# Kernel optimization log

Measured on AMD Instinct MI355X. Metric: run time of the kernel, lower is better.

Reference implementation:

```python
import jax, jax.numpy as jnp
import numpy as np

S, B, H, NH = 2048, 1, 1024, 16
HD = H // NH  # 64
NEG = float(np.finfo(np.float16).min)  # masked_fill value, matches torch.finfo(torch.float16).min


def setup_inputs() -> dict:
    key = jax.random.key(0)
    ks = jax.random.split(key, 9)
    w = lambda k: jax.random.normal(k, (H, H), jnp.float32) * 0.02
    b = lambda k: jax.random.normal(k, (H,), jnp.float32) * 0.01
    # causal (left-to-right) boolean mask, True = keep
    mask = jnp.tril(jnp.ones((S, S), dtype=bool))[None, None]  # [1,1,S,S]
    return {
        "hidden_states": jax.random.normal(ks[0], (S, B, H), jnp.float32),
        "Wq": w(ks[1]), "bq": b(ks[2]),
        "Wk": w(ks[3]), "bk": b(ks[4]),
        "Wv": w(ks[5]), "bv": b(ks[6]),
        "Wo": w(ks[7]), "bo": b(ks[8]),
        "attention_mask": mask,
    }


def reference(hidden_states, Wq, bq, Wk, bk, Wv, bv, Wo, bo, attention_mask):
    s, bsz, h = hidden_states.shape
    norm = float(np.sqrt(HD))
    # QKV projections (nn.Linear: x @ W.T + b), reshape to [S, B, NH, HD]
    q = (hidden_states @ Wq.T + bq).reshape(s, bsz, NH, HD) / norm
    k = (hidden_states @ Wk.T + bk).reshape(s, bsz, NH, HD)
    v = (hidden_states @ Wv.T + bv).reshape(s, bsz, NH, HD)
    # scores: [B, NH, S_q, S_kv] (baddbmm equivalent)
    scores = jnp.einsum('sbhd,tbhd->bhst', q, k)
    scores = jnp.where(attention_mask, scores, jnp.asarray(NEG, scores.dtype))
    # fp32 softmax, cast back to score dtype
    probs = jax.nn.softmax(scores.astype(jnp.float32), axis=-1).astype(scores.dtype)
    # context: [S, B, NH, HD] -> [S, B, H]
    ctx = jnp.einsum('bhst,tbhd->sbhd', probs, v).reshape(s, bsz, h)
    out = ctx @ Wo.T + bo
    return out
```

## Files before the change

kernel.cpp:

```cpp
#include <hip/hip_runtime.h>

typedef __attribute__((ext_vector_type(8))) short bf16x8;
typedef __attribute__((ext_vector_type(8))) unsigned short u16x8;
typedef __attribute__((ext_vector_type(4))) float f32x4;

#define GLDS16(SRC, DST) __builtin_amdgcn_global_load_lds( \
    (const __attribute__((address_space(1))) void*)(SRC),  \
    (__attribute__((address_space(3))) void*)(DST), 16, 0, 0)

__device__ __forceinline__ unsigned short f2bf(float f) {
  unsigned int u = __float_as_uint(f);
  u += 0x7FFFu + ((u >> 16) & 1u);
  return (unsigned short)(u >> 16);
}
__device__ __forceinline__ float bf2f(unsigned short u) {
  return __uint_as_float((unsigned int)u << 16);
}

__global__ void cvt_all(const float* __restrict__ hid,
                        const float* __restrict__ Wq, const float* __restrict__ Wk,
                        const float* __restrict__ Wv, const float* __restrict__ Wo,
                        const float* __restrict__ bq, const float* __restrict__ bk,
                        const float* __restrict__ bv,
                        unsigned short* __restrict__ hb, unsigned short* __restrict__ Wcat,
                        unsigned short* __restrict__ Wob, float* __restrict__ bcat) {
  const int H4 = 2048 * 1024 / 4, W4 = 1024 * 1024 / 4;
  int i = blockIdx.x * 256 + threadIdx.x;
  const float* src; unsigned short* dst; float scale = 1.0f; int j;
  if (i < H4)                { src = hid; dst = hb;                 j = i; }
  else if (i < H4 + W4)      { src = Wq;  dst = Wcat;               j = i - H4; scale = 0.125f; }
  else if (i < H4 + 2 * W4)  { src = Wk;  dst = Wcat + 1024 * 1024; j = i - H4 - W4; }
  else if (i < H4 + 3 * W4)  { src = Wv;  dst = Wcat + 2048 * 1024; j = i - H4 - 2 * W4; }
  else if (i < H4 + 4 * W4)  { src = Wo;  dst = Wob;                j = i - H4 - 3 * W4; }
  else {
    j = i - H4 - 4 * W4;
    int e = j * 4;
    const float* b = (e < 1024) ? bq : (e < 2048 ? bk + (-1024) : bv + (-2048));
    float4 v = *(const float4*)(b + e);
    if (e < 1024) { v.x *= 0.125f; v.y *= 0.125f; v.z *= 0.125f; v.w *= 0.125f; }
    ((float4*)bcat)[j] = v;
    return;
  }
  float4 v = ((const float4*)src)[j];
  ushort4 o;
  o.x = f2bf(v.x * scale); o.y = f2bf(v.y * scale);
  o.z = f2bf(v.z * scale); o.w = f2bf(v.w * scale);
  ((ushort4*)dst)[j] = o;
}

template <int BM, int BN, typename OutT>
__global__ __launch_bounds__(256) void gemm_bt(
    const unsigned short* __restrict__ A, const unsigned short* __restrict__ B,
    const float* __restrict__ bias, OutT* __restrict__ C,
    int M, int N, int K, int lda, int ldb, int ldc)
{
  constexpr int MREP = BM / 32, NREP = BN / 32;
  __shared__ __align__(16) unsigned short As[2][BM * 32];
  __shared__ __align__(16) unsigned short Bs[2][BN * 32];
  const int t = threadIdx.x;
  const int lane = t & 63;
  const int w = t >> 6;
  const int wm = w >> 1, wn = w & 1;
  const int lr = lane & 15, lk = lane >> 4;
  const int tm = blockIdx.y * BM, tn = blockIdx.x * BN;

  f32x4 acc[MREP][NREP];
#pragma unroll
  for (int m = 0; m < MREP; ++m)
#pragma unroll
    for (int n = 0; n < NREP; ++n) acc[m][n] = (f32x4){0.f, 0.f, 0.f, 0.f};

  const int ra0 = t >> 2;
  const int ka0 = (t & 3) << 3;
  const int ra1 = 64 + (t >> 2);
  const int lds0 = (t & 192) * 8;
  const int lds1 = (256 + (t & 192)) * 8;

  const int NT = K >> 5;
  GLDS16(A + (size_t)(tm + ra0) * lda + ka0, &As[0][lds0]);
  if constexpr (BM == 128) GLDS16(A + (size_t)(tm + ra1) * lda + ka0, &As[0][lds1]);
  GLDS16(B + (size_t)(tn + ra0) * ldb + ka0, &Bs[0][lds0]);
  if constexpr (BN == 128) GLDS16(B + (size_t)(tn + ra1) * ldb + ka0, &Bs[0][lds1]);
  __syncthreads();

  for (int kt = 0; kt < NT; ++kt) {
    const int cur = kt & 1, nxt = cur ^ 1;
    if (kt + 1 < NT) {
      const int k0 = (kt + 1) << 5;
      GLDS16(A + (size_t)(tm + ra0) * lda + k0 + ka0, &As[nxt][lds0]);
      if constexpr (BM == 128) GLDS16(A + (size_t)(tm + ra1) * lda + k0 + ka0, &As[nxt][lds1]);
      GLDS16(B + (size_t)(tn + ra0) * ldb + k0 + ka0, &Bs[nxt][lds0]);
      if constexpr (BN == 128) GLDS16(B + (size_t)(tn + ra1) * ldb + k0 + ka0, &Bs[nxt][lds1]);
    }
    bf16x8 af[MREP], bfv[NREP];
#pragma unroll
    for (int m = 0; m < MREP; ++m)
      af[m] = *(const bf16x8*)&As[cur][(wm * (BM / 2) + m * 16 + lr) * 32 + lk * 8];
#pragma unroll
    for (int n = 0; n < NREP; ++n)
      bfv[n] = *(const bf16x8*)&Bs[cur][(wn * (BN / 2) + n * 16 + lr) * 32 + lk * 8];
#pragma unroll
    for (int m = 0; m < MREP; ++m)
#pragma unroll
      for (int n = 0; n < NREP; ++n)
        acc[m][n] = __builtin_amdgcn_mfma_f32_16x16x32_bf16(af[m], bfv[n], acc[m][n], 0, 0, 0);
    __syncthreads();
  }

#pragma unroll
  for (int m = 0; m < MREP; ++m) {
    const int row0 = tm + wm * (BM / 2) + m * 16 + lk * 4;
#pragma unroll
    for (int n = 0; n < NREP; ++n) {
      const int col = tn + wn * (BN / 2) + n * 16 + lr;
      const float bb = bias ? bias[col] : 0.f;
#pragma unroll
      for (int r = 0; r < 4; ++r) {
        float v = acc[m][n][r] + bb;
        if constexpr (sizeof(OutT) == 2) {
          ((unsigned short*)C)[(size_t)(row0 + r) * ldc + col] = f2bf(v);
        } else {
          ((float*)C)[(size_t)(row0 + r) * ldc + col] = v;
        }
      }
    }
  }
}

__device__ __forceinline__ int slot_off(int qt) {
  int g = qt >> 3;
  return (g == 1) ? (qt - 8) * 2 : (g == 2) ? 16 + (qt - 16) * 3 : 40 + (qt - 24) * 4;
}

__global__ __launch_bounds__(256) void attn_fwd(const unsigned short* __restrict__ QKV,
                                                unsigned short* __restrict__ ctx,
                                                unsigned short* __restrict__ Opart,
                                                float* __restrict__ mlbuf)
{
  __shared__ __align__(16) unsigned short Ks[64 * 64];
  __shared__ __align__(16) unsigned short Vt[64 * 64];
  __shared__ __align__(16) unsigned int   Pl[4][16 * 36];

  const int t = threadIdx.x;
  const int lane = t & 63, w = t >> 6;
  const int lr = lane & 15, lk = lane >> 4;
  const int h = blockIdx.y;
  const int p = 79 - (int)blockIdx.x;
  int qt, c;
  if (p < 8)       { qt = p; c = 0; }
  else if (p < 24) { qt = 8 + ((p - 8) >> 1); c = (p - 8) & 1; }
  else if (p < 48) { int r = p - 24; qt = 16 + r / 3; c = r - (r / 3) * 3; }
  else             { int r = p - 48; qt = 24 + (r >> 2); c = r & 3; }
  const int nc = (qt >> 3) + 1;
  const int q0 = qt * 64;
  const size_t ldq = 3072;

  const unsigned short* qbase = QKV + (size_t)(q0 + w * 16 + lr) * ldq + h * 64;
  const bf16x8 qf0 = *(const bf16x8*)(qbase + lk * 8);
  const bf16x8 qf1 = *(const bf16x8*)(qbase + 32 + lk * 8);

  f32x4 acc[4];
#pragma unroll
  for (int d = 0; d < 4; ++d) acc[d] = (f32x4){0.f, 0.f, 0.f, 0.f};
  float mrun = -__builtin_inff(), lrun = 0.f;

  const int srow0 = t >> 3;
  const int srow1 = 32 + (t >> 3);
  const int sslot = t & 7;

  const unsigned short* kbase = QKV + 1024 + h * 64;
  const unsigned short* vbase = QKV + 2048 + h * 64;

  const int kt0 = c * 8;
  const int kt1 = (qt < kt0 + 7) ? qt : kt0 + 7;
  for (int kt = kt0; kt <= kt1; ++kt) {
    const int kv0 = kt * 64;
    __syncthreads();
    {
      const int c0 = (sslot ^ (srow0 & 7)) << 3;
      const int c1 = (sslot ^ (srow1 & 7)) << 3;
      GLDS16(kbase + (size_t)(kv0 + srow0) * ldq + c0, &Ks[(t & 192) * 8]);
      GLDS16(kbase + (size_t)(kv0 + srow1) * ldq + c1, &Ks[(256 + (t & 192)) * 8]);
    }
    {
      const bf16x8 v0 = *(const bf16x8*)(vbase + (size_t)(kv0 + srow0) * ldq + (sslot << 3));
      const bf16x8 v1 = *(const bf16x8*)(vbase + (size_t)(kv0 + srow1) * ldq + (sslot << 3));
      const int d0 = sslot << 3;
#pragma unroll
      for (int j = 0; j < 8; ++j) {
        const int d = d0 + j;
        const int key = (d ^ (d >> 3)) & 7;
        Vt[d * 64 + (((srow0 >> 3) ^ key) << 3) + (srow0 & 7)] = (unsigned short)v0[j];
        Vt[d * 64 + (((srow1 >> 3) ^ key) << 3) + (srow1 & 7)] = (unsigned short)v1[j];
      }
    }
    __syncthreads();

    f32x4 sacc[4];
#pragma unroll
    for (int sub = 0; sub < 4; ++sub) {
      const int krow = sub * 16 + lr;
      const int sw = krow & 7;
      const bf16x8 kf0 = *(const bf16x8*)&Ks[krow * 64 + ((lk ^ sw) << 3)];
      const bf16x8 kf1 = *(const bf16x8*)&Ks[krow * 64 + (((4 + lk) ^ sw) << 3)];
      f32x4 s = (f32x4){0.f, 0.f, 0.f, 0.f};
      s = __builtin_amdgcn_mfma_f32_16x16x32_bf16(kf0, qf0, s, 0, 0, 0);
      s = __builtin_amdgcn_mfma_f32_16x16x32_bf16(kf1, qf1, s, 0, 0, 0);
      sacc[sub] = s;
    }

    if (kt == qt) {
      const int qg = w * 16 + lr;
#pragma unroll
      for (int sub = 0; sub < 4; ++sub) {
#pragma unroll
        for (int r = 0; r < 4; ++r)
          if (sub * 16 + lk * 4 + r > qg) sacc[sub][r] = -__builtin_inff();
      }
    }

    float pm = -__builtin_inff();
#pragma unroll
    for (int sub = 0; sub < 4; ++sub)
#pragma unroll
      for (int r = 0; r < 4; ++r) pm = fmaxf(pm, sacc[sub][r]);
    pm = fmaxf(pm, __shfl_xor(pm, 16, 64));
    pm = fmaxf(pm, __shfl_xor(pm, 32, 64));
    const float mnew = fmaxf(mrun, pm);
    const float sc = __expf(mrun - mnew);
    lrun *= sc;
#pragma unroll
    for (int d = 0; d < 4; ++d) acc[d] *= sc;
    float pp[4][4]; float rs = 0.f;
#pragma unroll
    for (int sub = 0; sub < 4; ++sub)
#pragma unroll
      for (int r = 0; r < 4; ++r) { pp[sub][r] = __expf(sacc[sub][r] - mnew); rs += pp[sub][r]; }
    rs += __shfl_xor(rs, 16, 64);
    rs += __shfl_xor(rs, 32, 64);
    lrun += rs;
    mrun = mnew;

    unsigned int* prow = &Pl[w][lr * 36];
#pragma unroll
    for (int sub = 0; sub < 4; ++sub) {
#pragma unroll
      for (int j = 0; j < 2; ++j) {
        unsigned int pk;
        asm("v_cvt_pk_bf16_f32 %0, %1, %2" : "=v"(pk) : "v"(pp[sub][2 * j]), "v"(pp[sub][2 * j + 1]));
        prow[sub * 8 + lk * 2 + j] = pk;
      }
    }
    asm volatile("s_waitcnt lgkmcnt(0)" ::: "memory");
    __builtin_amdgcn_sched_barrier(0);

    const bf16x8 pb0 = *(const bf16x8*)&Pl[w][lr * 36 + lk * 4];
    const bf16x8 pb1 = *(const bf16x8*)&Pl[w][lr * 36 + 16 + lk * 4];
#pragma unroll
    for (int dsub = 0; dsub < 4; ++dsub) {
      const int dd = dsub * 16 + lr;
      const int key = (dd ^ (dd >> 3)) & 7;
      const bf16x8 bv0 = *(const bf16x8*)&Vt[dd * 64 + ((lk ^ key) << 3)];
      const bf16x8 bv1 = *(const bf16x8*)&Vt[dd * 64 + (((4 + lk) ^ key) << 3)];
      acc[dsub] = __builtin_amdgcn_mfma_f32_16x16x32_bf16(bv0, pb0, acc[dsub], 0, 0, 0);
      acc[dsub] = __builtin_amdgcn_mfma_f32_16x16x32_bf16(bv1, pb1, acc[dsub], 0, 0, 0);
    }
  }

  if (nc == 1) {
    const float inv = 1.0f / lrun;
#pragma unroll
    for (int dsub = 0; dsub < 4; ++dsub) {
      ushort4 o;
      o.x = f2bf(acc[dsub][0] * inv);
      o.y = f2bf(acc[dsub][1] * inv);
      o.z = f2bf(acc[dsub][2] * inv);
      o.w = f2bf(acc[dsub][3] * inv);
      *(ushort4*)&ctx[(size_t)(q0 + w * 16 + lr) * 1024 + h * 64 + dsub * 16 + lk * 4] = o;
    }
  } else {
    const int slot = h * 72 + slot_off(qt) + c;
    unsigned short* Op = Opart + (size_t)slot * 4096;
    const int ql = w * 16 + lr;
#pragma unroll
    for (int dsub = 0; dsub < 4; ++dsub) {
      ushort4 o;
      o.x = f2bf(acc[dsub][0]);
      o.y = f2bf(acc[dsub][1]);
      o.z = f2bf(acc[dsub][2]);
      o.w = f2bf(acc[dsub][3]);
      *(ushort4*)&Op[ql * 64 + dsub * 16 + lk * 4] = o;
    }
    if (lk == 0)
      *(float2*)&mlbuf[(slot * 64 + ql) * 2] = make_float2(mrun, lrun);
  }
}

template <int NC>
__device__ __forceinline__ void combine_body(const unsigned short* __restrict__ Opart,
                                             const float* __restrict__ mlbuf,
                                             unsigned short* __restrict__ ctx,
                                             int qt, int half, int h, int t) {
  const int q = half * 32 + (t >> 3);
  const int d0 = (t & 7) * 8;
  const int slot0 = h * 72 + slot_off(qt);
  float m[NC], l[NC];
#pragma unroll
  for (int c = 0; c < NC; ++c) {
    const float2 ml = *(const float2*)&mlbuf[((slot0 + c) * 64 + q) * 2];
    m[c] = ml.x; l[c] = ml.y;
  }
  float M = m[0];
#pragma unroll
  for (int c = 1; c < NC; ++c) M = fmaxf(M, m[c]);
  float wgt[NC], L = 0.f;
#pragma unroll
  for (int c = 0; c < NC; ++c) { wgt[c] = __expf(m[c] - M); L += wgt[c] * l[c]; }
  u16x8 v[NC];
#pragma unroll
  for (int c = 0; c < NC; ++c)
    v[c] = *(const u16x8*)&Opart[(size_t)(slot0 + c) * 4096 + q * 64 + d0];
  const float inv = 1.0f / L;
  u16x8 r;
#pragma unroll
  for (int j = 0; j < 8; ++j) {
    float o = 0.f;
#pragma unroll
    for (int c = 0; c < NC; ++c) o += wgt[c] * bf2f(v[c][j]);
    r[j] = f2bf(o * inv);
  }
  *(u16x8*)&ctx[(size_t)(qt * 64 + q) * 1024 + h * 64 + d0] = r;
}

__global__ __launch_bounds__(256) void attn_combine(const unsigned short* __restrict__ Opart,
                                                    const float* __restrict__ mlbuf,
                                                    unsigned short* __restrict__ ctx) {
  const int t = threadIdx.x;
  const int h = blockIdx.y;
  const int idx = blockIdx.x;
  const int g = idx >> 4;
  const int i = idx & 15;
  const int qt = 8 + g * 8 + (i >> 1);
  const int half = i & 1;
  if (g == 0)      combine_body<2>(Opart, mlbuf, ctx, qt, half, h, t);
  else if (g == 1) combine_body<3>(Opart, mlbuf, ctx, qt, half, h, t);
  else             combine_body<4>(Opart, mlbuf, ctx, qt, half, h, t);
}

extern "C" void kernel_launch(void* const* d_in, const int* in_sizes, int n_in,
                              void* d_out, int out_size, void* d_ws, size_t ws_size,
                              hipStream_t stream) {
  const float* hid = (const float*)d_in[0];
  const float* Wq  = (const float*)d_in[1];
  const float* bq  = (const float*)d_in[2];
  const float* Wk  = (const float*)d_in[3];
  const float* bk  = (const float*)d_in[4];
  const float* Wv  = (const float*)d_in[5];
  const float* bv  = (const float*)d_in[6];
  const float* Wo  = (const float*)d_in[7];
  const float* bo  = (const float*)d_in[8];
  float* out = (float*)d_out;

  char* ws = (char*)d_ws;
  unsigned short* hb   = (unsigned short*)(ws);
  unsigned short* Wcat = (unsigned short*)(ws + (4u  << 20));
  unsigned short* Wob  = (unsigned short*)(ws + (10u << 20));
  float*          bcat = (float*)         (ws + (12u << 20));
  unsigned short* QKV  = (unsigned short*)(ws + (13u << 20));
  unsigned short* ctx  = (unsigned short*)(ws + (25u << 20));
  unsigned short* Opart = (unsigned short*)(ws);
  float*          mlbuf = (float*)(ws + 9437184);

  cvt_all<<<6147, 256, 0, stream>>>(hid, Wq, Wk, Wv, Wo, bq, bk, bv,
                                    hb, Wcat, Wob, bcat);

  gemm_bt<64, 128, unsigned short><<<dim3(24, 32), 256, 0, stream>>>(
      hb, Wcat, bcat, QKV, 2048, 3072, 1024, 1024, 1024, 3072);

  attn_fwd<<<dim3(80, 16), 256, 0, stream>>>(QKV, ctx, Opart, mlbuf);

  attn_combine<<<dim3(48, 16), 256, 0, stream>>>(Opart, mlbuf, ctx);

  gemm_bt<64, 64, float><<<dim3(16, 32), 256, 0, stream>>>(
      ctx, Wob, bo, out, 2048, 1024, 1024, 1024, 1024, 1024);
}
```

Before: 86.13 us.

## Double-buffer K/V tiles and widen attention blocks to 128 query rows

The attention kernel now processes 128 query rows per block with 8 waves, halving the grid and doubling K/V tile reuse across waves. K and V tiles are double-buffered in LDS so the next tile's global loads overlap the current tile's MFMA work, which removes one barrier per iteration. MFMA sections are wrapped in s_setprio. The split-KV partition and combine indexing are remapped to the 128-row tiles. The costs are more LDS per block, fewer blocks in flight, and coarser load balance over the causal triangle.

```diff
diff --git a/kernel.cpp b/kernel.cpp
--- a/kernel.cpp
+++ b/kernel.cpp
@@ -128,94 +128,101 @@
 }
 
 __device__ __forceinline__ int slot_off(int qt) {
-  int g = qt >> 3;
-  return (g == 1) ? (qt - 8) * 2 : (g == 2) ? 16 + (qt - 16) * 3 : 40 + (qt - 24) * 4;
-}
-
-__global__ __launch_bounds__(256) void attn_fwd(const unsigned short* __restrict__ QKV,
-                                                unsigned short* __restrict__ ctx,
-                                                unsigned short* __restrict__ Opart,
-                                                float* __restrict__ mlbuf)
+  int g = qt >> 2;
+  return (g == 1) ? (qt - 4) * 2 : (g == 2) ? 8 + (qt - 8) * 3 : 20 + (qt - 12) * 4;
+}
+
+__global__ __launch_bounds__(512, 4) void attn_fwd(const unsigned short* __restrict__ QKV,
+                                                   unsigned short* __restrict__ ctx,
+                                                   unsigned short* __restrict__ Opart,
+                                                   float* __restrict__ mlbuf)
 {
-  __shared__ __align__(16) unsigned short Ks[64 * 64];
-  __shared__ __align__(16) unsigned short Vt[64 * 64];
-  __shared__ __align__(16) unsigned int   Pl[4][16 * 36];
+  __shared__ __align__(16) unsigned short Ks[2][64 * 64];
+  __shared__ __align__(16) unsigned short Vt[2][64 * 64];
+  __shared__ __align__(16) unsigned int   Pl[8][16 * 36];
 
   const int t = threadIdx.x;
   const int lane = t & 63, w = t >> 6;
   const int lr = lane & 15, lk = lane >> 4;
   const int h = blockIdx.y;
-  const int p = 79 - (int)blockIdx.x;
+  const int p = 39 - (int)blockIdx.x;
   int qt, c;
-  if (p < 8)       { qt = p; c = 0; }
-  else if (p < 24) { qt = 8 + ((p - 8) >> 1); c = (p - 8) & 1; }
-  else if (p < 48) { int r = p - 24; qt = 16 + r / 3; c = r - (r / 3) * 3; }
-  else             { int r = p - 48; qt = 24 + (r >> 2); c = r & 3; }
-  const int nc = (qt >> 3) + 1;
-  const int q0 = qt * 64;
+  if (p < 4)       { qt = p; c = 0; }
+  else if (p < 12) { qt = 4 + ((p - 4) >> 1); c = (p - 4) & 1; }
+  else if (p < 24) { int r = p - 12; qt = 8 + r / 3; c = r - (r / 3) * 3; }
+  else             { int r = p - 24; qt = 12 + (r >> 2); c = r & 3; }
+  const int nc = (qt >> 2) + 1;
+  const int q0 = qt * 128;
+  const int qd = 2 * qt + 1;
   const size_t ldq = 3072;
 
   const unsigned short* qbase = QKV + (size_t)(q0 + w * 16 + lr) * ldq + h * 64;
   const bf16x8 qf0 = *(const bf16x8*)(qbase + lk * 8);
   const bf16x8 qf1 = *(const bf16x8*)(qbase + 32 + lk * 8);
+  const int qglob = q0 + w * 16 + lr;
 
   f32x4 acc[4];
 #pragma unroll
   for (int d = 0; d < 4; ++d) acc[d] = (f32x4){0.f, 0.f, 0.f, 0.f};
   float mrun = -__builtin_inff(), lrun = 0.f;
 
-  const int srow0 = t >> 3;
-  const int srow1 = 32 + (t >> 3);
+  const int srow = t >> 3;
   const int sslot = t & 7;
+  const int scol = (sslot ^ (srow & 7)) << 3;
+  const int ldsb = (t & 448) * 8;
 
   const unsigned short* kbase = QKV + 1024 + h * 64;
   const unsigned short* vbase = QKV + 2048 + h * 64;
 
   const int kt0 = c * 8;
-  const int kt1 = (qt < kt0 + 7) ? qt : kt0 + 7;
+  const int kt1 = (qd < kt0 + 7) ? qd : kt0 + 7;
+
+  {
+    const int kv0 = kt0 * 64;
+    GLDS16(kbase + (size_t)(kv0 + srow) * ldq + scol, &Ks[0][ldsb]);
+    const bf16x8 v0 = *(const bf16x8*)(vbase + (size_t)(kv0 + srow) * ldq + (sslot << 3));
+    const int d0 = sslot << 3;
+#pragma unroll
+    for (int j = 0; j < 8; ++j) {
+      const int d = d0 + j;
+      const int key = (d ^ (d >> 3)) & 7;
+      Vt[0][d * 64 + (((srow >> 3) ^ key) << 3) + (srow & 7)] = (unsigned short)v0[j];
+    }
+  }
+  __syncthreads();
+
+  int cur = 0;
   for (int kt = kt0; kt <= kt1; ++kt) {
+    const bool more = kt < kt1;
+    bf16x8 vnxt;
+    if (more) {
+      const int kvn = (kt + 1) * 64;
+      GLDS16(kbase + (size_t)(kvn + srow) * ldq + scol, &Ks[cur ^ 1][ldsb]);
+      vnxt = *(const bf16x8*)(vbase + (size_t)(kvn + srow) * ldq + (sslot << 3));
+    }
+
     const int kv0 = kt * 64;
-    __syncthreads();
-    {
-      const int c0 = (sslot ^ (srow0 & 7)) << 3;
-      const int c1 = (sslot ^ (srow1 & 7)) << 3;
-      GLDS16(kbase + (size_t)(kv0 + srow0) * ldq + c0, &Ks[(t & 192) * 8]);
-      GLDS16(kbase + (size_t)(kv0 + srow1) * ldq + c1, &Ks[(256 + (t & 192)) * 8]);
-    }
-    {
-      const bf16x8 v0 = *(const bf16x8*)(vbase + (size_t)(kv0 + srow0) * ldq + (sslot << 3));
-      const bf16x8 v1 = *(const bf16x8*)(vbase + (size_t)(kv0 + srow1) * ldq + (sslot << 3));
-      const int d0 = sslot << 3;
-#pragma unroll
-      for (int j = 0; j < 8; ++j) {
-        const int d = d0 + j;
-        const int key = (d ^ (d >> 3)) & 7;
-        Vt[d * 64 + (((srow0 >> 3) ^ key) << 3) + (srow0 & 7)] = (unsigned short)v0[j];
-        Vt[d * 64 + (((srow1 >> 3) ^ key) << 3) + (srow1 & 7)] = (unsigned short)v1[j];
-      }
-    }
-    __syncthreads();
-
     f32x4 sacc[4];
+    __builtin_amdgcn_s_setprio(1);
 #pragma unroll
     for (int sub = 0; sub < 4; ++sub) {
       const int krow = sub * 16 + lr;
       const int sw = krow & 7;
-      const bf16x8 kf0 = *(const bf16x8*)&Ks[krow * 64 + ((lk ^ sw) << 3)];
-      const bf16x8 kf1 = *(const bf16x8*)&Ks[krow * 64 + (((4 + lk) ^ sw) << 3)];
+      const bf16x8 kf0 = *(const bf16x8*)&Ks[cur][krow * 64 + ((lk ^ sw) << 3)];
+      const bf16x8 kf1 = *(const bf16x8*)&Ks[cur][krow * 64 + (((4 + lk) ^ sw) << 3)];
       f32x4 s = (f32x4){0.f, 0.f, 0.f, 0.f};
       s = __builtin_amdgcn_mfma_f32_16x16x32_bf16(kf0, qf0, s, 0, 0, 0);
       s = __builtin_amdgcn_mfma_f32_16x16x32_bf16(kf1, qf1, s, 0, 0, 0);
       sacc[sub] = s;
     }
-
-    if (kt == qt) {
-      const int qg = w * 16 + lr;
+    __builtin_amdgcn_s_setprio(0);
+
+    if (kt + 1 >= qd) {
 #pragma unroll
       for (int sub = 0; sub < 4; ++sub) {
 #pragma unroll
         for (int r = 0; r < 4; ++r)
-          if (sub * 16 + lk * 4 + r > qg) sacc[sub][r] = -__builtin_inff();
+          if (kv0 + sub * 16 + lk * 4 + r > qglob) sacc[sub][r] = -__builtin_inff();
       }
     }
 
@@ -256,14 +263,29 @@
 
     const bf16x8 pb0 = *(const bf16x8*)&Pl[w][lr * 36 + lk * 4];
     const bf16x8 pb1 = *(const bf16x8*)&Pl[w][lr * 36 + 16 + lk * 4];
+    __builtin_amdgcn_s_setprio(1);
 #pragma unroll
     for (int dsub = 0; dsub < 4; ++dsub) {
       const int dd = dsub * 16 + lr;
       const int key = (dd ^ (dd >> 3)) & 7;
-      const bf16x8 bv0 = *(const bf16x8*)&Vt[dd * 64 + ((lk ^ key) << 3)];
-      const bf16x8 bv1 = *(const bf16x8*)&Vt[dd * 64 + (((4 + lk) ^ key) << 3)];
+      const bf16x8 bv0 = *(const bf16x8*)&Vt[cur][dd * 64 + ((lk ^ key) << 3)];
+      const bf16x8 bv1 = *(const bf16x8*)&Vt[cur][dd * 64 + (((4 + lk) ^ key) << 3)];
       acc[dsub] = __builtin_amdgcn_mfma_f32_16x16x32_bf16(bv0, pb0, acc[dsub], 0, 0, 0);
       acc[dsub] = __builtin_amdgcn_mfma_f32_16x16x32_bf16(bv1, pb1, acc[dsub], 0, 0, 0);
+    }
+    __builtin_amdgcn_s_setprio(0);
+
+    if (more) {
+      const int d0 = sslot << 3;
+      const int nxt = cur ^ 1;
+#pragma unroll
+      for (int j = 0; j < 8; ++j) {
+        const int d = d0 + j;
+        const int key = (d ^ (d >> 3)) & 7;
+        Vt[nxt][d * 64 + (((srow >> 3) ^ key) << 3) + (srow & 7)] = (unsigned short)vnxt[j];
+      }
+      __syncthreads();
+      cur = nxt;
     }
   }
 
@@ -276,11 +298,11 @@
       o.y = f2bf(acc[dsub][1] * inv);
       o.z = f2bf(acc[dsub][2] * inv);
       o.w = f2bf(acc[dsub][3] * inv);
-      *(ushort4*)&ctx[(size_t)(q0 + w * 16 + lr) * 1024 + h * 64 + dsub * 16 + lk * 4] = o;
+      *(ushort4*)&ctx[(size_t)qglob * 1024 + h * 64 + dsub * 16 + lk * 4] = o;
     }
   } else {
-    const int slot = h * 72 + slot_off(qt) + c;
-    unsigned short* Op = Opart + (size_t)slot * 4096;
+    const int slot = h * 36 + slot_off(qt) + c;
+    unsigned short* Op = Opart + (size_t)slot * 8192;
     const int ql = w * 16 + lr;
 #pragma unroll
     for (int dsub = 0; dsub < 4; ++dsub) {
@@ -292,7 +314,7 @@
       *(ushort4*)&Op[ql * 64 + dsub * 16 + lk * 4] = o;
     }
     if (lk == 0)
-      *(float2*)&mlbuf[(slot * 64 + ql) * 2] = make_float2(mrun, lrun);
+      *(float2*)&mlbuf[(slot * 128 + ql) * 2] = make_float2(mrun, lrun);
   }
 }
 
@@ -300,14 +322,14 @@
 __device__ __forceinline__ void combine_body(const unsigned short* __restrict__ Opart,
                                              const float* __restrict__ mlbuf,
                                              unsigned short* __restrict__ ctx,
-                                             int qt, int half, int h, int t) {
-  const int q = half * 32 + (t >> 3);
+                                             int qt, int quarter, int h, int t) {
+  const int q = quarter * 32 + (t >> 3);
   const int d0 = (t & 7) * 8;
-  const int slot0 = h * 72 + slot_off(qt);
+  const int slot0 = h * 36 + slot_off(qt);
   float m[NC], l[NC];
 #pragma unroll
   for (int c = 0; c < NC; ++c) {
-    const float2 ml = *(const float2*)&mlbuf[((slot0 + c) * 64 + q) * 2];
+    const float2 ml = *(const float2*)&mlbuf[((slot0 + c) * 128 + q) * 2];
     m[c] = ml.x; l[c] = ml.y;
   }
   float M = m[0];
@@ -319,7 +341,7 @@
   u16x8 v[NC];
 #pragma unroll
   for (int c = 0; c < NC; ++c)
-    v[c] = *(const u16x8*)&Opart[(size_t)(slot0 + c) * 4096 + q * 64 + d0];
+    v[c] = *(const u16x8*)&Opart[(size_t)(slot0 + c) * 8192 + q * 64 + d0];
   const float inv = 1.0f / L;
   u16x8 r;
 #pragma unroll
@@ -329,7 +351,7 @@
     for (int c = 0; c < NC; ++c) o += wgt[c] * bf2f(v[c][j]);
     r[j] = f2bf(o * inv);
   }
-  *(u16x8*)&ctx[(size_t)(qt * 64 + q) * 1024 + h * 64 + d0] = r;
+  *(u16x8*)&ctx[(size_t)(qt * 128 + q) * 1024 + h * 64 + d0] = r;
 }
 
 __global__ __launch_bounds__(256) void attn_combine(const unsigned short* __restrict__ Opart,
@@ -340,11 +362,11 @@
   const int idx = blockIdx.x;
   const int g = idx >> 4;
   const int i = idx & 15;
-  const int qt = 8 + g * 8 + (i >> 1);
-  const int half = i & 1;
-  if (g == 0)      combine_body<2>(Opart, mlbuf, ctx, qt, half, h, t);
-  else if (g == 1) combine_body<3>(Opart, mlbuf, ctx, qt, half, h, t);
-  else             combine_body<4>(Opart, mlbuf, ctx, qt, half, h, t);
+  const int qt = 4 + g * 4 + (i >> 2);
+  const int quarter = i & 3;
+  if (g == 0)      combine_body<2>(Opart, mlbuf, ctx, qt, quarter, h, t);
+  else if (g == 1) combine_body<3>(Opart, mlbuf, ctx, qt, quarter, h, t);
+  else             combine_body<4>(Opart, mlbuf, ctx, qt, quarter, h, t);
 }
 
 extern "C" void kernel_launch(void* const* d_in, const int* in_sizes, int n_in,
@@ -377,7 +399,7 @@
   gemm_bt<64, 128, unsigned short><<<dim3(24, 32), 256, 0, stream>>>(
       hb, Wcat, bcat, QKV, 2048, 3072, 1024, 1024, 1024, 3072);
 
-  attn_fwd<<<dim3(80, 16), 256, 0, stream>>>(QKV, ctx, Opart, mlbuf);
+  attn_fwd<<<dim3(40, 16), 512, 0, stream>>>(QKV, ctx, Opart, mlbuf);
 
   attn_combine<<<dim3(48, 16), 256, 0, stream>>>(Opart, mlbuf, ctx);
 
```

New measurement: 86.24 us. No clear change (+0.1%).

## Prefetch next K/V tile into registers and double-buffer V in LDS

Applied to the files above, without the earlier changes.

The attention kernel stops staging K through LDS. Each lane now loads its K MFMA fragments straight from global memory into registers, and the next K and V tiles are prefetched during the current tile's compute. V gets a double buffer in LDS, so each iteration needs one barrier instead of two. It also adds s_setprio around the MFMA blocks and a launch-bounds occupancy hint of 3 waves per SIMD. In exchange, register pressure rises from holding both the current and next K fragments, and the K loads are redundant across the four waves.

```diff
diff --git a/kernel.cpp b/kernel.cpp
--- a/kernel.cpp
+++ b/kernel.cpp
@@ -132,13 +132,12 @@
   return (g == 1) ? (qt - 8) * 2 : (g == 2) ? 16 + (qt - 16) * 3 : 40 + (qt - 24) * 4;
 }
 
-__global__ __launch_bounds__(256) void attn_fwd(const unsigned short* __restrict__ QKV,
-                                                unsigned short* __restrict__ ctx,
-                                                unsigned short* __restrict__ Opart,
-                                                float* __restrict__ mlbuf)
+__global__ __launch_bounds__(256, 3) void attn_fwd(const unsigned short* __restrict__ QKV,
+                                                   unsigned short* __restrict__ ctx,
+                                                   unsigned short* __restrict__ Opart,
+                                                   float* __restrict__ mlbuf)
 {
-  __shared__ __align__(16) unsigned short Ks[64 * 64];
-  __shared__ __align__(16) unsigned short Vt[64 * 64];
+  __shared__ __align__(16) unsigned short Vt[2][64 * 64];
   __shared__ __align__(16) unsigned int   Pl[4][16 * 36];
 
   const int t = threadIdx.x;
@@ -170,44 +169,60 @@
 
   const unsigned short* kbase = QKV + 1024 + h * 64;
   const unsigned short* vbase = QKV + 2048 + h * 64;
+  const unsigned short* kfp = kbase + (size_t)lr * ldq + lk * 8;
 
   const int kt0 = c * 8;
   const int kt1 = (qt < kt0 + 7) ? qt : kt0 + 7;
+
+  bf16x8 kc0[4], kc1[4];
+
+  {
+    const int kv0 = kt0 * 64;
+#pragma unroll
+    for (int sub = 0; sub < 4; ++sub) {
+      const unsigned short* kp = kfp + (size_t)(kv0 + sub * 16) * ldq;
+      kc0[sub] = *(const bf16x8*)kp;
+      kc1[sub] = *(const bf16x8*)(kp + 32);
+    }
+    const bf16x8 v0 = *(const bf16x8*)(vbase + (size_t)(kv0 + srow0) * ldq + (sslot << 3));
+    const bf16x8 v1 = *(const bf16x8*)(vbase + (size_t)(kv0 + srow1) * ldq + (sslot << 3));
+    const int d0 = sslot << 3;
+#pragma unroll
+    for (int j = 0; j < 8; ++j) {
+      const int d = d0 + j;
+      const int key = (d ^ (d >> 3)) & 7;
+      Vt[0][d * 64 + (((srow0 >> 3) ^ key) << 3) + (srow0 & 7)] = (unsigned short)v0[j];
+      Vt[0][d * 64 + (((srow1 >> 3) ^ key) << 3) + (srow1 & 7)] = (unsigned short)v1[j];
+    }
+  }
+  __syncthreads();
+
+  int cur = 0;
   for (int kt = kt0; kt <= kt1; ++kt) {
-    const int kv0 = kt * 64;
-    __syncthreads();
-    {
-      const int c0 = (sslot ^ (srow0 & 7)) << 3;
-      const int c1 = (sslot ^ (srow1 & 7)) << 3;
-      GLDS16(kbase + (size_t)(kv0 + srow0) * ldq + c0, &Ks[(t & 192) * 8]);
-      GLDS16(kbase + (size_t)(kv0 + srow1) * ldq + c1, &Ks[(256 + (t & 192)) * 8]);
-    }
-    {
-      const bf16x8 v0 = *(const bf16x8*)(vbase + (size_t)(kv0 + srow0) * ldq + (sslot << 3));
-      const bf16x8 v1 = *(const bf16x8*)(vbase + (size_t)(kv0 + srow1) * ldq + (sslot << 3));
-      const int d0 = sslot << 3;
-#pragma unroll
-      for (int j = 0; j < 8; ++j) {
-        const int d = d0 + j;
-        const int key = (d ^ (d >> 3)) & 7;
-        Vt[d * 64 + (((srow0 >> 3) ^ key) << 3) + (srow0 & 7)] = (unsigned short)v0[j];
-        Vt[d * 64 + (((srow1 >> 3) ^ key) << 3) + (srow1 & 7)] = (unsigned short)v1[j];
+    const bool more = kt < kt1;
+    bf16x8 kn0[4], kn1[4], vn0, vn1;
+    if (more) {
+      const int kvn = (kt + 1) * 64;
+#pragma unroll
+      for (int sub = 0; sub < 4; ++sub) {
+        const unsigned short* kp = kfp + (size_t)(kvn + sub * 16) * ldq;
+        kn0[sub] = *(const bf16x8*)kp;
+        kn1[sub] = *(const bf16x8*)(kp + 32);
       }
-    }
-    __syncthreads();
+      vn0 = *(const bf16x8*)(vbase + (size_t)(kvn + srow0) * ldq + (sslot << 3));
+      vn1 = *(const bf16x8*)(vbase + (size_t)(kvn + srow1) * ldq + (sslot << 3));
+    }
 
     f32x4 sacc[4];
+    __builtin_amdgcn_s_setprio(1);
 #pragma unroll
     for (int sub = 0; sub < 4; ++sub) {
-      const int krow = sub * 16 + lr;
-      const int sw = krow & 7;
-      const bf16x8 kf0 = *(const bf16x8*)&Ks[krow * 64 + ((lk ^ sw) << 3)];
-      const bf16x8 kf1 = *(const bf16x8*)&Ks[krow * 64 + (((4 + lk) ^ sw) << 3)];
       f32x4 s = (f32x4){0.f, 0.f, 0.f, 0.f};
-      s = __builtin_amdgcn_mfma_f32_16x16x32_bf16(kf0, qf0, s, 0, 0, 0);
-      s = __builtin_amdgcn_mfma_f32_16x16x32_bf16(kf1, qf1, s, 0, 0, 0);
+      s = __builtin_amdgcn_mfma_f32_16x16x32_bf16(kc0[sub], qf0, s, 0, 0, 0);
+      s = __builtin_amdgcn_mfma_f32_16x16x32_bf16(kc1[sub], qf1, s, 0, 0, 0);
       sacc[sub] = s;
     }
+    __builtin_amdgcn_s_setprio(0);
 
     if (kt == qt) {
       const int qg = w * 16 + lr;
@@ -256,14 +271,32 @@
 
     const bf16x8 pb0 = *(const bf16x8*)&Pl[w][lr * 36 + lk * 4];
     const bf16x8 pb1 = *(const bf16x8*)&Pl[w][lr * 36 + 16 + lk * 4];
+    __builtin_amdgcn_s_setprio(1);
 #pragma unroll
     for (int dsub = 0; dsub < 4; ++dsub) {
       const int dd = dsub * 16 + lr;
       const int key = (dd ^ (dd >> 3)) & 7;
-      const bf16x8 bv0 = *(const bf16x8*)&Vt[dd * 64 + ((lk ^ key) << 3)];
-      const bf16x8 bv1 = *(const bf16x8*)&Vt[dd * 64 + (((4 + lk) ^ key) << 3)];
+      const bf16x8 bv0 = *(const bf16x8*)&Vt[cur][dd * 64 + ((lk ^ key) << 3)];
+      const bf16x8 bv1 = *(const bf16x8*)&Vt[cur][dd * 64 + (((4 + lk) ^ key) << 3)];
       acc[dsub] = __builtin_amdgcn_mfma_f32_16x16x32_bf16(bv0, pb0, acc[dsub], 0, 0, 0);
       acc[dsub] = __builtin_amdgcn_mfma_f32_16x16x32_bf16(bv1, pb1, acc[dsub], 0, 0, 0);
+    }
+    __builtin_amdgcn_s_setprio(0);
+
+    if (more) {
+      const int d0 = sslot << 3;
+      const int nxt = cur ^ 1;
+#pragma unroll
+      for (int j = 0; j < 8; ++j) {
+        const int d = d0 + j;
+        const int key = (d ^ (d >> 3)) & 7;
+        Vt[nxt][d * 64 + (((srow0 >> 3) ^ key) << 3) + (srow0 & 7)] = (unsigned short)vn0[j];
+        Vt[nxt][d * 64 + (((srow1 >> 3) ^ key) << 3) + (srow1 & 7)] = (unsigned short)vn1[j];
+      }
+      __syncthreads();
+      cur = nxt;
+#pragma unroll
+      for (int sub = 0; sub < 4; ++sub) { kc0[sub] = kn0[sub]; kc1[sub] = kn1[sub]; }
     }
   }
 
```

Result: slower. 106.7 us (+23.8%).

## Deepen GEMM K-tile with XOR-swizzled LDS and lazily rescale softmax

Applied to the files above, without the earlier changes.

The projection GEMM now stages 64-wide K slices instead of 32, with an XOR swizzle on the LDS column index to avoid bank conflicts. Each barrier therefore covers twice as many MFMAs. The attention kernel also skips the online-softmax rescale when the new block max stays within 8 of the running max across the wave, saving exp and multiply work. The costs are double the LDS use, which may lower occupancy, and p values up to e^8 before normalisation, which fit comfortably in fp32 but add some risk to bf16 precision.

```diff
diff --git a/kernel.cpp b/kernel.cpp
--- a/kernel.cpp
+++ b/kernel.cpp
@@ -55,8 +55,9 @@
     int M, int N, int K, int lda, int ldb, int ldc)
 {
   constexpr int MREP = BM / 32, NREP = BN / 32;
-  __shared__ __align__(16) unsigned short As[2][BM * 32];
-  __shared__ __align__(16) unsigned short Bs[2][BN * 32];
+  constexpr int AI = BM / 32, BI = BN / 32;
+  __shared__ __align__(16) unsigned short As[2][BM * 64];
+  __shared__ __align__(16) unsigned short Bs[2][BN * 64];
   const int t = threadIdx.x;
   const int lane = t & 63;
   const int w = t >> 6;
@@ -70,40 +71,50 @@
 #pragma unroll
     for (int n = 0; n < NREP; ++n) acc[m][n] = (f32x4){0.f, 0.f, 0.f, 0.f};
 
-  const int ra0 = t >> 2;
-  const int ka0 = (t & 3) << 3;
-  const int ra1 = 64 + (t >> 2);
-  const int lds0 = (t & 192) * 8;
-  const int lds1 = (256 + (t & 192)) * 8;
-
-  const int NT = K >> 5;
-  GLDS16(A + (size_t)(tm + ra0) * lda + ka0, &As[0][lds0]);
-  if constexpr (BM == 128) GLDS16(A + (size_t)(tm + ra1) * lda + ka0, &As[0][lds1]);
-  GLDS16(B + (size_t)(tn + ra0) * ldb + ka0, &Bs[0][lds0]);
-  if constexpr (BN == 128) GLDS16(B + (size_t)(tn + ra1) * ldb + ka0, &Bs[0][lds1]);
+  const int srow = t >> 3;
+  const int scol = ((t & 7) ^ (srow & 7)) << 3;
+  const int ldsb = (t & 192) * 8;
+
+  const int NT = K >> 6;
+#pragma unroll
+  for (int i = 0; i < AI; ++i)
+    GLDS16(A + (size_t)(tm + i * 32 + srow) * lda + scol, &As[0][i * 2048 + ldsb]);
+#pragma unroll
+  for (int i = 0; i < BI; ++i)
+    GLDS16(B + (size_t)(tn + i * 32 + srow) * ldb + scol, &Bs[0][i * 2048 + ldsb]);
   __syncthreads();
 
   for (int kt = 0; kt < NT; ++kt) {
     const int cur = kt & 1, nxt = cur ^ 1;
     if (kt + 1 < NT) {
-      const int k0 = (kt + 1) << 5;
-      GLDS16(A + (size_t)(tm + ra0) * lda + k0 + ka0, &As[nxt][lds0]);
-      if constexpr (BM == 128) GLDS16(A + (size_t)(tm + ra1) * lda + k0 + ka0, &As[nxt][lds1]);
-      GLDS16(B + (size_t)(tn + ra0) * ldb + k0 + ka0, &Bs[nxt][lds0]);
-      if constexpr (BN == 128) GLDS16(B + (size_t)(tn + ra1) * ldb + k0 + ka0, &Bs[nxt][lds1]);
-    }
-    bf16x8 af[MREP], bfv[NREP];
-#pragma unroll
-    for (int m = 0; m < MREP; ++m)
-      af[m] = *(const bf16x8*)&As[cur][(wm * (BM / 2) + m * 16 + lr) * 32 + lk * 8];
-#pragma unroll
-    for (int n = 0; n < NREP; ++n)
-      bfv[n] = *(const bf16x8*)&Bs[cur][(wn * (BN / 2) + n * 16 + lr) * 32 + lk * 8];
-#pragma unroll
-    for (int m = 0; m < MREP; ++m)
-#pragma unroll
-      for (int n = 0; n < NREP; ++n)
-        acc[m][n] = __builtin_amdgcn_mfma_f32_16x16x32_bf16(af[m], bfv[n], acc[m][n], 0, 0, 0);
+      const int k0 = (kt + 1) << 6;
+#pragma unroll
+      for (int i = 0; i < AI; ++i)
+        GLDS16(A + (size_t)(tm + i * 32 + srow) * lda + k0 + scol, &As[nxt][i * 2048 + ldsb]);
+#pragma unroll
+      for (int i = 0; i < BI; ++i)
+        GLDS16(B + (size_t)(tn + i * 32 + srow) * ldb + k0 + scol, &Bs[nxt][i * 2048 + ldsb]);
+    }
+    bf16x8 af[MREP][2], bfv[NREP][2];
+#pragma unroll
+    for (int m = 0; m < MREP; ++m) {
+      const int ra = wm * (BM / 2) + m * 16 + lr, r7 = ra & 7;
+      af[m][0] = *(const bf16x8*)&As[cur][ra * 64 + ((lk ^ r7) << 3)];
+      af[m][1] = *(const bf16x8*)&As[cur][ra * 64 + (((4 + lk) ^ r7) << 3)];
+    }
+#pragma unroll
+    for (int n = 0; n < NREP; ++n) {
+      const int rb = wn * (BN / 2) + n * 16 + lr, r7 = rb & 7;
+      bfv[n][0] = *(const bf16x8*)&Bs[cur][rb * 64 + ((lk ^ r7) << 3)];
+      bfv[n][1] = *(const bf16x8*)&Bs[cur][rb * 64 + (((4 + lk) ^ r7) << 3)];
+    }
+#pragma unroll
+    for (int kk = 0; kk < 2; ++kk)
+#pragma unroll
+      for (int m = 0; m < MREP; ++m)
+#pragma unroll
+        for (int n = 0; n < NREP; ++n)
+          acc[m][n] = __builtin_amdgcn_mfma_f32_16x16x32_bf16(af[m][kk], bfv[n][kk], acc[m][n], 0, 0, 0);
     __syncthreads();
   }
 
@@ -226,20 +237,22 @@
       for (int r = 0; r < 4; ++r) pm = fmaxf(pm, sacc[sub][r]);
     pm = fmaxf(pm, __shfl_xor(pm, 16, 64));
     pm = fmaxf(pm, __shfl_xor(pm, 32, 64));
-    const float mnew = fmaxf(mrun, pm);
-    const float sc = __expf(mrun - mnew);
-    lrun *= sc;
-#pragma unroll
-    for (int d = 0; d < 4; ++d) acc[d] *= sc;
+    if (!__all(pm <= mrun + 8.0f)) {
+      const float mnew = fmaxf(mrun, pm);
+      const float sc = __expf(mrun - mnew);
+      lrun *= sc;
+#pragma unroll
+      for (int d = 0; d < 4; ++d) acc[d] *= sc;
+      mrun = mnew;
+    }
     float pp[4][4]; float rs = 0.f;
 #pragma unroll
     for (int sub = 0; sub < 4; ++sub)
 #pragma unroll
-      for (int r = 0; r < 4; ++r) { pp[sub][r] = __expf(sacc[sub][r] - mnew); rs += pp[sub][r]; }
+      for (int r = 0; r < 4; ++r) { pp[sub][r] = __expf(sacc[sub][r] - mrun); rs += pp[sub][r]; }
     rs += __shfl_xor(rs, 16, 64);
     rs += __shfl_xor(rs, 32, 64);
     lrun += rs;
-    mrun = mnew;
 
     unsigned int* prow = &Pl[w][lr * 36];
 #pragma unroll
```

New measurement: 78.22 us. 9.2% less time.
